# Kernel tuning notes

Hardware: AMD Instinct MI355X
Metric: run time of the kernel (lower is better)

The kernel has to match this reference:

```python
import jax, jax.numpy as jnp
import numpy as np

IN_CH = 64
OUT_CH = 64
MODES = 16
BATCH, H, W = 16, 128, 128


def setup_inputs() -> dict:
    key = jax.random.key(0)
    k1, k2, k3 = jax.random.split(key, 3)
    scale = 1.0 / (IN_CH * OUT_CH)
    x = jax.random.normal(k1, (BATCH, H, W, IN_CH), dtype=jnp.float32)
    weights_real = (scale * jax.random.normal(k2, (IN_CH, OUT_CH, MODES, MODES))).astype(jnp.float32)
    weights_imag = (scale * jax.random.normal(k3, (IN_CH, OUT_CH, MODES, MODES))).astype(jnp.float32)
    return {"x": x, "weights_real": weights_real, "weights_imag": weights_imag}


def reference(x, weights_real, weights_imag):
    # x: (b, h, w, c_in)
    b, h, w, _ = x.shape
    modes = weights_real.shape[-1]
    out_ch = weights_real.shape[1]

    xc = jnp.transpose(x, (0, 3, 1, 2))               # (b, c_in, h, w)
    x_ft = jnp.fft.rfft2(xc, norm="ortho")           # (b, c_in, h, w//2+1) complex64

    # Complex spectral weights; the torch double loop over (i, j) is exactly
    # a per-mode channel contraction over the low-frequency block.
    Wc = (weights_real + 1j * weights_imag).astype(jnp.complex64)
    out_modes = jnp.einsum("bixy,ioxy->boxy", x_ft[:, :, :modes, :modes], Wc)

    out_ft = jnp.zeros((b, out_ch, h, w // 2 + 1), dtype=jnp.complex64)
    out_ft = out_ft.at[:, :, :modes, :modes].set(out_modes)

    y = jnp.fft.irfft2(out_ft, s=(h, w), norm="ortho")  # (b, c_out, h, w)
    return jnp.transpose(y, (0, 2, 3, 1))                # (b, h, w, c_out)
```

## Files before the change

### kernel.cpp

```cpp
#include <hip/hip_runtime.h>

#define NB 16
#define NH 128
#define NW 128
#define NC 64
#define NO 64
#define NM 16

#define OFF_WTR  0
#define OFF_WTI  (OFF_WTR + 1048576)
#define OFF_AR   (OFF_WTI + 1048576)
#define OFF_AI   (OFF_AR + 2097152)
#define OFF_XR   (OFF_AI + 2097152)
#define OFF_XI   (OFF_XR + 262144)
#define OFF_OR   (OFF_XI + 262144)
#define OFF_OI   (OFF_OR + 262144)

#define R2F 0.70710678118654752f

constexpr float CQ[33] = {
  1.000000000f, 0.998795456f, 0.995184727f, 0.989176510f,
  0.980785280f, 0.970031253f, 0.956940336f, 0.941544065f,
  0.923879533f, 0.903989293f, 0.881921264f, 0.857728610f,
  0.831469612f, 0.803207531f, 0.773010453f, 0.740951125f,
  0.707106781f, 0.671558955f, 0.634393284f, 0.595699304f,
  0.555570233f, 0.514102744f, 0.471396737f, 0.427555093f,
  0.382683432f, 0.336889853f, 0.290284677f, 0.242980180f,
  0.195090322f, 0.146730474f, 0.098017140f, 0.049067674f,
  0.000000000f };

__host__ __device__ constexpr float twcos(int t) {
  t &= 127;
  return (t <= 32) ? CQ[t] : (t < 64) ? -CQ[64 - t] : (t <= 96) ? -CQ[t - 64] : CQ[128 - t];
}
__host__ __device__ constexpr float twsin(int t) { return twcos(t + 96); }

template<int T>
__device__ __forceinline__ void caccN_t(float gr, float gi, float& ar, float& ai) {
  constexpr int t = T & 127;
  if constexpr (t == 0)       { ar += gr; ai += gi; }
  else if constexpr (t == 64) { ar -= gr; ai -= gi; }
  else if constexpr (t == 32) { ar += gi; ai -= gr; }
  else if constexpr (t == 96) { ar -= gi; ai += gr; }
  else {
    constexpr float c = twcos(t), s = twsin(t);
    ar = fmaf(gr, c, fmaf(gi, s, ar));
    ai = fmaf(gi, c, fmaf(-gr, s, ai));
  }
}
template<int T>
__device__ __forceinline__ void caccP_t(float gr, float gi, float& ar, float& ai) {
  constexpr int t = T & 127;
  if constexpr (t == 0)       { ar += gr; ai += gi; }
  else if constexpr (t == 64) { ar -= gr; ai -= gi; }
  else if constexpr (t == 32) { ar -= gi; ai += gr; }
  else if constexpr (t == 96) { ar += gi; ai -= gr; }
  else {
    constexpr float c = twcos(t), s = twsin(t);
    ar = fmaf(gr, c, fmaf(-gi, s, ar));
    ai = fmaf(gi, c, fmaf(gr, s, ai));
  }
}
template<int T>
__device__ __forceinline__ void crotN_t(float& ar, float& ai) {
  constexpr int t = T & 127;
  if constexpr (t == 0) {}
  else if constexpr (t == 64) { ar = -ar; ai = -ai; }
  else if constexpr (t == 32) { const float r = ar; ar = ai; ai = -r; }
  else if constexpr (t == 96) { const float r = ar; ar = -ai; ai = r; }
  else {
    constexpr float c = twcos(t), s = twsin(t);
    const float r = ar;
    ar = fmaf(r, c, ai * s);
    ai = fmaf(ai, c, -r * s);
  }
}
template<int T>
__device__ __forceinline__ void crotP_t(float& ar, float& ai) {
  constexpr int t = T & 127;
  if constexpr (t == 0) {}
  else if constexpr (t == 64) { ar = -ar; ai = -ai; }
  else if constexpr (t == 32) { const float r = ar; ar = -ai; ai = r; }
  else if constexpr (t == 96) { const float r = ar; ar = ai;  ai = -r; }
  else {
    constexpr float c = twcos(t), s = twsin(t);
    const float r = ar;
    ar = fmaf(r, c, -(ai * s));
    ai = fmaf(ai, c, r * s);
  }
}

__global__ __launch_bounds__(256) void k_wt(const float* __restrict__ wre,
                                            const float* __restrict__ wim,
                                            float* __restrict__ wtr,
                                            float* __restrict__ wti) {
  __shared__ float buf[64 * 257];
  const int i = blockIdx.x & 63;
  const float* src = (blockIdx.x < 64) ? wre : wim;
  float* dst       = (blockIdx.x < 64) ? wtr : wti;
  const float* s = src + (size_t)i * 16384;
  for (int t = threadIdx.x; t < 16384; t += 256) {
    int o = t >> 8, kk = t & 255;
    buf[o * 257 + kk] = s[t];
  }
  __syncthreads();
  for (int t = threadIdx.x; t < 16384; t += 256) {
    int kk = t >> 6, o = t & 63;
    dst[(size_t)kk * 4096 + i * 64 + o] = buf[o * 257 + kk];
  }
}

template<int K>
__device__ __forceinline__ void k1_zeroT(float (&Tr)[16], float (&Ti)[16]) {
  if constexpr (K < 16) { Tr[K] = 0.f; Ti[K] = 0.f; k1_zeroT<K + 1>(Tr, Ti); }
}
template<int K, int P0>
__device__ __forceinline__ void k1_initR(float (&Rr)[16], float (&Ri)[16]) {
  if constexpr (K < 16) {
    constexpr int t = (K * P0) & 127;
    Rr[K] = twcos(t);
    Ri[K] = -twsin(t);
    k1_initR<K + 1, P0>(Rr, Ri);
  }
}
template<int W1>
__device__ __forceinline__ void k1_ld8(const float* xp, int w0, float (&v)[8]) {
  if constexpr (W1 < 8) {
    v[W1] = xp[(W1 * 16 + w0) * NC];
    k1_ld8<W1 + 1>(xp, w0, v);
  }
}
template<int W1>
__device__ __forceinline__ void k1_cp8(float (&a)[8], const float (&b)[8]) {
  if constexpr (W1 < 8) { a[W1] = b[W1]; k1_cp8<W1 + 1>(a, b); }
}
template<int KY>
__device__ __forceinline__ void k1_acc(float g0r, float g4r, float g1r, float g1i,
                                       float g2r, float g2i, float g3r, float g3i,
                                       float (&Tr)[16], float (&Ti)[16],
                                       float (&Rr)[16], float (&Ri)[16]) {
  if constexpr (KY < 16) {
    constexpr int p = KY & 7;
    if constexpr (p == 0 || p == 4) {
      const float gr = (p == 0) ? g0r : g4r;
      Tr[KY] = fmaf(gr, Rr[KY], Tr[KY]);
      Ti[KY] = fmaf(gr, Ri[KY], Ti[KY]);
    } else {
      float gr, gi;
      if constexpr (p == 1)      { gr = g1r; gi = g1i; }
      else if constexpr (p == 2) { gr = g2r; gi = g2i; }
      else if constexpr (p == 3) { gr = g3r; gi = g3i; }
      else if constexpr (p == 5) { gr = g3r; gi = -g3i; }
      else if constexpr (p == 6) { gr = g2r; gi = -g2i; }
      else                       { gr = g1r; gi = -g1i; }
      Tr[KY] = fmaf(gr, Rr[KY], fmaf(-gi, Ri[KY], Tr[KY]));
      Ti[KY] = fmaf(gr, Ri[KY], fmaf( gi, Rr[KY], Ti[KY]));
    }
    crotN_t<KY>(Rr[KY], Ri[KY]);
    k1_acc<KY + 1>(g0r, g4r, g1r, g1i, g2r, g2i, g3r, g3i, Tr, Ti, Rr, Ri);
  }
}
template<int K>
__device__ __forceinline__ void k1_ldswr(float* p, const float (&Tr)[16], const float (&Ti)[16]) {
  if constexpr (K < 16) {
    p[K * 64]        = Tr[K];
    p[(16 + K) * 64] = Ti[K];
    k1_ldswr<K + 1>(p, Tr, Ti);
  }
}
template<int K>
__device__ __forceinline__ void k1_ldsadd(const float* p, float (&Tr)[16], float (&Ti)[16]) {
  if constexpr (K < 16) {
    Tr[K] += p[K * 64];
    Ti[K] += p[(16 + K) * 64];
    k1_ldsadd<K + 1>(p, Tr, Ti);
  }
}
template<int KY>
__device__ __forceinline__ void k1_store(float* t1r, float* t1i,
                                         const float (&Tr)[16], const float (&Ti)[16]) {
  if constexpr (KY < 16) {
    t1r[(size_t)KY * (NH * NC)] = Tr[KY];
    t1i[(size_t)KY * (NH * NC)] = Ti[KY];
    k1_store<KY + 1>(t1r, t1i, Tr, Ti);
  }
}

__global__ __launch_bounds__(256, 4) void k1_wdft(const float* __restrict__ x,
                                                  float* __restrict__ t1r,
                                                  float* __restrict__ t1i) {
  __shared__ float lds[2][32][64];
  const int wv   = threadIdx.x >> 6;
  const int lane = threadIdx.x & 63;
  const int sq   = wv >> 1;
  const int half = wv & 1;
  const int slab = blockIdx.x * 2 + sq;
  const float* xp = x + (size_t)slab * (NW * NC) + lane;
  float Tr[16], Ti[16], Rr[16], Ri[16];
  k1_zeroT<0>(Tr, Ti);
  if (half == 0) k1_initR<0, 0>(Rr, Ri);
  else           k1_initR<0, 8>(Rr, Ri);
  float xv[8], nx[8];
  k1_ld8<0>(xp, half * 8, xv);
  for (int it = 0; it < 8; ++it) {
    const int w0 = half * 8 + it;
    if (it < 7) k1_ld8<0>(xp, w0 + 1, nx);
    const float s0 = xv[0] + xv[4], d0 = xv[0] - xv[4];
    const float s1 = xv[1] + xv[5], d1 = xv[1] - xv[5];
    const float s2 = xv[2] + xv[6], d2 = xv[2] - xv[6];
    const float s3 = xv[3] + xv[7], d3 = xv[3] - xv[7];
    const float e0 = s0 + s2, e1 = s0 - s2;
    const float f0 = s1 + s3, f1 = s1 - s3;
    const float u = R2F * (d1 - d3), v = R2F * (d1 + d3);
    const float g0r = e0 + f0;
    const float g4r = e0 - f0;
    const float g1r = d0 + u, g1i = -(d2 + v);
    const float g2r = e1,     g2i = -f1;
    const float g3r = d0 - u, g3i = d2 - v;
    k1_acc<0>(g0r, g4r, g1r, g1i, g2r, g2i, g3r, g3i, Tr, Ti, Rr, Ri);
    k1_cp8<0>(xv, nx);
  }
  float* lp = &lds[sq][0][lane];
  if (half) k1_ldswr<0>(lp, Tr, Ti);
  __syncthreads();
  if (!half) {
    k1_ldsadd<0>(lp, Tr, Ti);
    const int b = slab >> 7, h = slab & 127;
    const size_t base = ((size_t)b * 2048 + h) * NC + lane;
    k1_store<0>(t1r + base, t1i + base, Tr, Ti);
  }
}

template<int K>
__device__ __forceinline__ void k2a_zero(float (&Ar)[16], float (&Ai)[16]) {
  if constexpr (K < 16) { Ar[K] = 0.f; Ai[K] = 0.f; k2a_zero<K + 1>(Ar, Ai); }
}
template<int KX, int J>
__device__ __forceinline__ void k2a_kx(float re, float im, float (&Ar)[16], float (&Ai)[16]) {
  if constexpr (KX < 16) {
    caccN_t<(KX * J) & 127>(re, im, Ar[KX], Ai[KX]);
    k2a_kx<KX + 1, J>(re, im, Ar, Ai);
  }
}
template<int J>
__device__ __forceinline__ void k2a_j(const float* pr, const float* pi,
                                      float (&Ar)[16], float (&Ai)[16]) {
  if constexpr (J < 8) {
    const float re = pr[J * NC];
    const float im = pi[J * NC];
    k2a_kx<0, J>(re, im, Ar, Ai);
    k2a_j<J + 1>(pr, pi, Ar, Ai);
  }
}
template<int G, int KX>
__device__ __forceinline__ void k2a_rotg(float (&Ar)[16], float (&Ai)[16]) {
  if constexpr (KX < 16) {
    crotN_t<(8 * KX * G) & 127>(Ar[KX], Ai[KX]);
    k2a_rotg<G, KX + 1>(Ar, Ai);
  }
}
template<int KX>
__device__ __forceinline__ void k2a_ldsw(float* pr, float* pi,
                                         const float (&Ar)[16], const float (&Ai)[16]) {
  if constexpr (KX < 16) {
    pr[KX * 64] = Ar[KX]; pi[KX * 64] = Ai[KX];
    k2a_ldsw<KX + 1>(pr, pi, Ar, Ai);
  }
}
template<int KX>
__device__ __forceinline__ void k2a_ldsa(float* pr, float* pi,
                                         const float (&Ar)[16], const float (&Ai)[16]) {
  if constexpr (KX < 16) {
    pr[KX * 64] += Ar[KX]; pi[KX * 64] += Ai[KX];
    k2a_ldsa<KX + 1>(pr, pi, Ar, Ai);
  }
}

__global__ __launch_bounds__(1024, 4) void k2a_hdft(const float* __restrict__ t1r,
                                                    const float* __restrict__ t1i,
                                                    float* __restrict__ xre,
                                                    float* __restrict__ xim) {
  __shared__ float lpr[8][16][64];
  __shared__ float lpi[8][16][64];
  const int bk   = blockIdx.x;
  const int q    = threadIdx.x >> 6;
  const int lane = threadIdx.x & 63;
  const float* pr = t1r + (size_t)bk * (NH * NC) + (q * 8) * NC + lane;
  const float* pi = t1i + (size_t)bk * (NH * NC) + (q * 8) * NC + lane;
  float Ar[16], Ai[16];
  k2a_zero<0>(Ar, Ai);
  k2a_j<0>(pr, pi, Ar, Ai);
  switch (q) {
    case 1:  k2a_rotg<1, 0>(Ar, Ai);  break;
    case 2:  k2a_rotg<2, 0>(Ar, Ai);  break;
    case 3:  k2a_rotg<3, 0>(Ar, Ai);  break;
    case 4:  k2a_rotg<4, 0>(Ar, Ai);  break;
    case 5:  k2a_rotg<5, 0>(Ar, Ai);  break;
    case 6:  k2a_rotg<6, 0>(Ar, Ai);  break;
    case 7:  k2a_rotg<7, 0>(Ar, Ai);  break;
    case 8:  k2a_rotg<8, 0>(Ar, Ai);  break;
    case 9:  k2a_rotg<9, 0>(Ar, Ai);  break;
    case 10: k2a_rotg<10, 0>(Ar, Ai); break;
    case 11: k2a_rotg<11, 0>(Ar, Ai); break;
    case 12: k2a_rotg<12, 0>(Ar, Ai); break;
    case 13: k2a_rotg<13, 0>(Ar, Ai); break;
    case 14: k2a_rotg<14, 0>(Ar, Ai); break;
    case 15: k2a_rotg<15, 0>(Ar, Ai); break;
    default: break;
  }
  float* wpr = &lpr[q & 7][0][lane];
  float* wpi = &lpi[q & 7][0][lane];
  if (q < 8) k2a_ldsw<0>(wpr, wpi, Ar, Ai);
  __syncthreads();
  if (q >= 8) k2a_ldsa<0>(wpr, wpi, Ar, Ai);
  __syncthreads();
  const int kx = threadIdx.x >> 6;
  const int i  = threadIdx.x & 63;
  float sr = 0.f, si = 0.f;
#pragma unroll
  for (int p = 0; p < 8; ++p) { sr += lpr[p][kx][i]; si += lpi[p][kx][i]; }
  const int b = bk >> 4, ky = bk & 15;
  const size_t idx = (size_t)(kx * NM + ky) * (NB * NC) + b * NC + i;
  xre[idx] = sr;
  xim[idx] = si;
}

__global__ __launch_bounds__(512, 2) void k2b_mix(const float* __restrict__ xre,
                                                  const float* __restrict__ xim,
                                                  const float* __restrict__ wtr,
                                                  const float* __restrict__ wti,
                                                  float* __restrict__ ore,
                                                  float* __restrict__ oim) {
  __shared__ __align__(16) float lwr[4096], lwi[4096];
  __shared__ __align__(16) float lxr[1024], lxi[1024];
  const int kk = blockIdx.x;
  for (int t = threadIdx.x; t < 4096; t += 512) {
    lwr[t] = wtr[(size_t)kk * 4096 + t];
    lwi[t] = wti[(size_t)kk * 4096 + t];
  }
  for (int t = threadIdx.x; t < 1024; t += 512) {
    lxr[t] = xre[(size_t)kk * 1024 + t];
    lxi[t] = xim[(size_t)kk * 1024 + t];
  }
  __syncthreads();
  const int o  = threadIdx.x & 63;
  const int bq = threadIdx.x >> 6;
  float accr[2] = {0, 0}, acci[2] = {0, 0};
  for (int iq = 0; iq < 16; ++iq) {
    float xrv[2][4], xiv[2][4];
#pragma unroll
    for (int p = 0; p < 2; ++p) {
      const int b = bq * 2 + p;
      float4 vr = ((const float4*)lxr)[b * 16 + iq];
      float4 vi = ((const float4*)lxi)[b * 16 + iq];
      xrv[p][0] = vr.x; xrv[p][1] = vr.y; xrv[p][2] = vr.z; xrv[p][3] = vr.w;
      xiv[p][0] = vi.x; xiv[p][1] = vi.y; xiv[p][2] = vi.z; xiv[p][3] = vi.w;
    }
#pragma unroll
    for (int j = 0; j < 4; ++j) {
      const int i2 = iq * 4 + j;
      const float wr = lwr[i2 * 64 + o];
      const float wi = lwi[i2 * 64 + o];
#pragma unroll
      for (int p = 0; p < 2; ++p) {
        accr[p] = fmaf(xrv[p][j], wr, fmaf(-xiv[p][j], wi, accr[p]));
        acci[p] = fmaf(xrv[p][j], wi, fmaf(xiv[p][j], wr, acci[p]));
      }
    }
  }
#pragma unroll
  for (int p = 0; p < 2; ++p) {
    const int b = bq * 2 + p;
    ore[(size_t)kk * 1024 + b * 64 + o] = accr[p];
    oim[(size_t)kk * 1024 + b * 64 + o] = acci[p];
  }
}

__global__ __launch_bounds__(256, 2) void k3_hidft(const float* __restrict__ ore,
                                                   const float* __restrict__ oim,
                                                   float* __restrict__ t2r,
                                                   float* __restrict__ t2i) {
  const int b = blockIdx.x >> 5, hq = blockIdx.x & 31;
  const int q = threadIdx.x >> 6, lane = threadIdx.x & 63;
  const int ky0 = q * 4;
  float sc[4], ss[4];
  {
    const int h0 = 4 * hq;
    float wr = 1.f, wi = 0.f;
    if (h0 & 4)  crotP_t<4>(wr, wi);
    if (h0 & 8)  crotP_t<8>(wr, wi);
    if (h0 & 16) crotP_t<16>(wr, wi);
    if (h0 & 32) crotP_t<32>(wr, wi);
    if (h0 & 64) crotP_t<64>(wr, wi);
    sc[0] = wr; ss[0] = wi;
    crotP_t<1>(wr, wi); sc[1] = wr; ss[1] = wi;
    crotP_t<1>(wr, wi); sc[2] = wr; ss[2] = wi;
    crotP_t<1>(wr, wi); sc[3] = wr; ss[3] = wi;
  }
  float Rr[4] = {1.f, 1.f, 1.f, 1.f}, Ri[4] = {0.f, 0.f, 0.f, 0.f};
  float tr[4][4], ti[4][4];
#pragma unroll
  for (int j = 0; j < 4; ++j)
#pragma unroll
    for (int k = 0; k < 4; ++k) { tr[j][k] = 0.f; ti[j][k] = 0.f; }
  const size_t obase = (size_t)b * NO + lane;
  for (int kx = 0; kx < 16; ++kx) {
    float orv[4], oiv[4];
#pragma unroll
    for (int k = 0; k < 4; ++k) {
      const size_t idx = (size_t)(kx * 16 + ky0 + k) * (NB * NO) + obase;
      orv[k] = ore[idx];
      oiv[k] = oim[idx];
    }
#pragma unroll
    for (int j = 0; j < 4; ++j)
#pragma unroll
      for (int k = 0; k < 4; ++k) {
        tr[j][k] = fmaf(orv[k], Rr[j], fmaf(-oiv[k], Ri[j], tr[j][k]));
        ti[j][k] = fmaf(orv[k], Ri[j], fmaf( oiv[k], Rr[j], ti[j][k]));
      }
#pragma unroll
    for (int j = 0; j < 4; ++j) {
      const float nr = fmaf(Rr[j], sc[j], -(Ri[j] * ss[j]));
      const float ni = fmaf(Rr[j], ss[j], Ri[j] * sc[j]);
      Rr[j] = nr; Ri[j] = ni;
    }
  }
#pragma unroll
  for (int j = 0; j < 4; ++j) {
    const int h = hq * 4 + j;
#pragma unroll
    for (int k = 0; k < 4; ++k) {
      const int ky = ky0 + k;
      const float scale = (ky == 0 ? 1.0f : 2.0f) * (1.0f / 16384.0f);
      const size_t idx = ((size_t)(b * NH + h) * NM + ky) * NO + lane;
      t2r[idx] = tr[j][k] * scale;
      t2i[idx] = ti[j][k] * scale;
    }
  }
}

template<int KY>
__device__ __forceinline__ void k5_load(const float* pr, const float* pi,
                                        float (&Tr)[16], float (&Ti)[16]) {
  if constexpr (KY < 16) {
    Tr[KY] = pr[KY * NO];
    Ti[KY] = pi[KY * NO];
    k5_load<KY + 1>(pr, pi, Tr, Ti);
  }
}
template<int KY, int W0>
__device__ __forceinline__ void k5_u(const float (&Tr)[16], const float (&Ti)[16],
                                     float (&Ur)[8], float (&Ui)[8]) {
  if constexpr (KY < 16) {
    caccP_t<(KY * W0) & 127>(Tr[KY], Ti[KY], Ur[KY & 7], Ui[KY & 7]);
    k5_u<KY + 1, W0>(Tr, Ti, Ur, Ui);
  }
}
template<int P>
__device__ __forceinline__ void k5_uzero(float (&Ur)[8], float (&Ui)[8]) {
  if constexpr (P < 8) { Ur[P] = 0.f; Ui[P] = 0.f; k5_uzero<P + 1>(Ur, Ui); }
}
template<int W0, int W0END>
__device__ __forceinline__ void k5_w0(const float (&Tr)[16], const float (&Ti)[16],
                                      float* yp) {
  if constexpr (W0 < W0END) {
    float Ur[8], Ui[8];
    k5_uzero<0>(Ur, Ui);
    k5_u<0, W0>(Tr, Ti, Ur, Ui);
    const float A  = Ur[0], B = Ur[4];
    const float Cr = Ur[2] + Ur[6], Ci = Ui[2] - Ui[6];
    const float Dr = Ur[1] + Ur[7], Di = Ui[1] - Ui[7];
    const float Er = Ur[3] + Ur[5], Ei = Ui[3] - Ui[5];
    const float P = A + B, M = A - B;
    const float DE = Dr + Er, IE = Di - Ei;
    const float X1 = R2F * ((Dr - Di) - (Er + Ei));
    const float X3 = R2F * ((Dr + Di) - (Er - Ei));
    const float MmC = M - Ci, MpC = M + Ci, PpC = P + Cr, PmC = P - Cr;
    yp[(0 * 16 + W0) * NO] = PpC + DE;
    yp[(4 * 16 + W0) * NO] = PpC - DE;
    yp[(2 * 16 + W0) * NO] = PmC - IE;
    yp[(6 * 16 + W0) * NO] = PmC + IE;
    yp[(1 * 16 + W0) * NO] = MmC + X1;
    yp[(5 * 16 + W0) * NO] = MmC - X1;
    yp[(3 * 16 + W0) * NO] = MpC - X3;
    yp[(7 * 16 + W0) * NO] = MpC + X3;
    k5_w0<W0 + 1, W0END>(Tr, Ti, yp);
  }
}

__global__ __launch_bounds__(256, 4) void k5_widft(const float* __restrict__ t2r,
                                                   const float* __restrict__ t2i,
                                                   float* __restrict__ y) {
  const int wv   = threadIdx.x >> 6;
  const int lane = threadIdx.x & 63;
  const int sq   = wv >> 1;
  const int half = wv & 1;
  const int slab = blockIdx.x * 2 + sq;
  const float* pr = t2r + (size_t)slab * (NM * NO) + lane;
  const float* pi = t2i + (size_t)slab * (NM * NO) + lane;
  float Tr[16], Ti[16];
  k5_load<0>(pr, pi, Tr, Ti);
  float* yp = y + (size_t)slab * (NW * NO) + lane;
  if (half == 0) k5_w0<0, 8>(Tr, Ti, yp);
  else           k5_w0<8, 16>(Tr, Ti, yp);
}

extern "C" void kernel_launch(void* const* d_in, const int* in_sizes, int n_in,
                              void* d_out, int out_size, void* d_ws, size_t ws_size,
                              hipStream_t stream) {
  const float* x   = (const float*)d_in[0];
  const float* wre = (const float*)d_in[1];
  const float* wim = (const float*)d_in[2];
  float* ws  = (float*)d_ws;
  float* wtr = ws + OFF_WTR;
  float* wti = ws + OFF_WTI;
  float* ar  = ws + OFF_AR;
  float* ai  = ws + OFF_AI;
  float* xr  = ws + OFF_XR;
  float* xi  = ws + OFF_XI;
  float* orr = ws + OFF_OR;
  float* oii = ws + OFF_OI;
  float* y   = (float*)d_out;

  k_wt<<<128, 256, 0, stream>>>(wre, wim, wtr, wti);
  k1_wdft<<<1024, 256, 0, stream>>>(x, ar, ai);
  k2a_hdft<<<NB * NM, 1024, 0, stream>>>(ar, ai, xr, xi);
  k2b_mix<<<NM * NM, 512, 0, stream>>>(xr, xi, wtr, wti, orr, oii);
  k3_hidft<<<512, 256, 0, stream>>>(orr, oii, ar, ai);
  k5_widft<<<1024, 256, 0, stream>>>(ar, ai, y);
}
```

Baseline: 155.6 us.

## Fuse inverse H/W DFT kernels and drop separate weight transpose

```diff
diff --git a/kernel.cpp b/kernel.cpp
--- a/kernel.cpp
+++ b/kernel.cpp
@@ -7,9 +7,7 @@
 #define NO 64
 #define NM 16
 
-#define OFF_WTR  0
-#define OFF_WTI  (OFF_WTR + 1048576)
-#define OFF_AR   (OFF_WTI + 1048576)
+#define OFF_AR   0
 #define OFF_AI   (OFF_AR + 2097152)
 #define OFF_XR   (OFF_AI + 2097152)
 #define OFF_XI   (OFF_XR + 262144)
@@ -87,26 +85,6 @@
     const float r = ar;
     ar = fmaf(r, c, -(ai * s));
     ai = fmaf(ai, c, r * s);
-  }
-}
-
-__global__ __launch_bounds__(256) void k_wt(const float* __restrict__ wre,
-                                            const float* __restrict__ wim,
-                                            float* __restrict__ wtr,
-                                            float* __restrict__ wti) {
-  __shared__ float buf[64 * 257];
-  const int i = blockIdx.x & 63;
-  const float* src = (blockIdx.x < 64) ? wre : wim;
-  float* dst       = (blockIdx.x < 64) ? wtr : wti;
-  const float* s = src + (size_t)i * 16384;
-  for (int t = threadIdx.x; t < 16384; t += 256) {
-    int o = t >> 8, kk = t & 255;
-    buf[o * 257 + kk] = s[t];
-  }
-  __syncthreads();
-  for (int t = threadIdx.x; t < 16384; t += 256) {
-    int kk = t >> 6, o = t & 63;
-    dst[(size_t)kk * 4096 + i * 64 + o] = buf[o * 257 + kk];
   }
 }
 
@@ -327,16 +305,16 @@
 
 __global__ __launch_bounds__(512, 2) void k2b_mix(const float* __restrict__ xre,
                                                   const float* __restrict__ xim,
-                                                  const float* __restrict__ wtr,
-                                                  const float* __restrict__ wti,
+                                                  const float* __restrict__ wre,
+                                                  const float* __restrict__ wim,
                                                   float* __restrict__ ore,
                                                   float* __restrict__ oim) {
   __shared__ __align__(16) float lwr[4096], lwi[4096];
   __shared__ __align__(16) float lxr[1024], lxi[1024];
   const int kk = blockIdx.x;
   for (int t = threadIdx.x; t < 4096; t += 512) {
-    lwr[t] = wtr[(size_t)kk * 4096 + t];
-    lwi[t] = wti[(size_t)kk * 4096 + t];
+    lwr[t] = wre[(size_t)t * 256 + kk];
+    lwi[t] = wim[(size_t)t * 256 + kk];
   }
   for (int t = threadIdx.x; t < 1024; t += 512) {
     lxr[t] = xre[(size_t)kk * 1024 + t];
@@ -376,77 +354,51 @@
   }
 }
 
-__global__ __launch_bounds__(256, 2) void k3_hidft(const float* __restrict__ ore,
-                                                   const float* __restrict__ oim,
-                                                   float* __restrict__ t2r,
-                                                   float* __restrict__ t2i) {
-  const int b = blockIdx.x >> 5, hq = blockIdx.x & 31;
-  const int q = threadIdx.x >> 6, lane = threadIdx.x & 63;
-  const int ky0 = q * 4;
-  float sc[4], ss[4];
-  {
-    const int h0 = 4 * hq;
-    float wr = 1.f, wi = 0.f;
-    if (h0 & 4)  crotP_t<4>(wr, wi);
-    if (h0 & 8)  crotP_t<8>(wr, wi);
-    if (h0 & 16) crotP_t<16>(wr, wi);
-    if (h0 & 32) crotP_t<32>(wr, wi);
-    if (h0 & 64) crotP_t<64>(wr, wi);
-    sc[0] = wr; ss[0] = wi;
-    crotP_t<1>(wr, wi); sc[1] = wr; ss[1] = wi;
-    crotP_t<1>(wr, wi); sc[2] = wr; ss[2] = wi;
-    crotP_t<1>(wr, wi); sc[3] = wr; ss[3] = wi;
-  }
-  float Rr[4] = {1.f, 1.f, 1.f, 1.f}, Ri[4] = {0.f, 0.f, 0.f, 0.f};
-  float tr[4][4], ti[4][4];
-#pragma unroll
-  for (int j = 0; j < 4; ++j)
-#pragma unroll
-    for (int k = 0; k < 4; ++k) { tr[j][k] = 0.f; ti[j][k] = 0.f; }
-  const size_t obase = (size_t)b * NO + lane;
-  for (int kx = 0; kx < 16; ++kx) {
-    float orv[4], oiv[4];
-#pragma unroll
-    for (int k = 0; k < 4; ++k) {
-      const size_t idx = (size_t)(kx * 16 + ky0 + k) * (NB * NO) + obase;
-      orv[k] = ore[idx];
-      oiv[k] = oim[idx];
-    }
-#pragma unroll
-    for (int j = 0; j < 4; ++j)
-#pragma unroll
-      for (int k = 0; k < 4; ++k) {
-        tr[j][k] = fmaf(orv[k], Rr[j], fmaf(-oiv[k], Ri[j], tr[j][k]));
-        ti[j][k] = fmaf(orv[k], Ri[j], fmaf( oiv[k], Rr[j], ti[j][k]));
-      }
-#pragma unroll
-    for (int j = 0; j < 4; ++j) {
-      const float nr = fmaf(Rr[j], sc[j], -(Ri[j] * ss[j]));
-      const float ni = fmaf(Rr[j], ss[j], Ri[j] * sc[j]);
-      Rr[j] = nr; Ri[j] = ni;
-    }
-  }
-#pragma unroll
-  for (int j = 0; j < 4; ++j) {
-    const int h = hq * 4 + j;
-#pragma unroll
-    for (int k = 0; k < 4; ++k) {
-      const int ky = ky0 + k;
-      const float scale = (ky == 0 ? 1.0f : 2.0f) * (1.0f / 16384.0f);
-      const size_t idx = ((size_t)(b * NH + h) * NM + ky) * NO + lane;
-      t2r[idx] = tr[j][k] * scale;
-      t2i[idx] = ti[j][k] * scale;
-    }
-  }
-}
-
-template<int KY>
-__device__ __forceinline__ void k5_load(const float* pr, const float* pi,
+template<int K>
+__device__ __forceinline__ void k35_zero(float (&Tr)[16], float (&Ti)[16]) {
+  if constexpr (K < 16) { Tr[K] = 0.f; Ti[K] = 0.f; k35_zero<K + 1>(Tr, Ti); }
+}
+template<int KY, int KYEND>
+__device__ __forceinline__ void k35_ld(const float* orp, const float* oip,
+                                       float (&orv)[16], float (&oiv)[16]) {
+  if constexpr (KY < KYEND) {
+    orv[KY] = orp[KY * (NB * NO)];
+    oiv[KY] = oip[KY * (NB * NO)];
+    k35_ld<KY + 1, KYEND>(orp, oip, orv, oiv);
+  }
+}
+template<int KY, int KYEND>
+__device__ __forceinline__ void k35_acc(const float (&orv)[16], const float (&oiv)[16],
+                                        float Rr, float Ri,
                                         float (&Tr)[16], float (&Ti)[16]) {
-  if constexpr (KY < 16) {
-    Tr[KY] = pr[KY * NO];
-    Ti[KY] = pi[KY * NO];
-    k5_load<KY + 1>(pr, pi, Tr, Ti);
+  if constexpr (KY < KYEND) {
+    Tr[KY] = fmaf(orv[KY], Rr, fmaf(-oiv[KY], Ri, Tr[KY]));
+    Ti[KY] = fmaf(orv[KY], Ri, fmaf( oiv[KY], Rr, Ti[KY]));
+    k35_acc<KY + 1, KYEND>(orv, oiv, Rr, Ri, Tr, Ti);
+  }
+}
+template<int K>
+__device__ __forceinline__ void k35_ldswr(float* p, const float (&Tr)[16], const float (&Ti)[16]) {
+  if constexpr (K < 16) {
+    p[K * 64]        = Tr[K];
+    p[(16 + K) * 64] = Ti[K];
+    k35_ldswr<K + 1>(p, Tr, Ti);
+  }
+}
+template<int K>
+__device__ __forceinline__ void k35_ldsadd(const float* p, float (&Tr)[16], float (&Ti)[16]) {
+  if constexpr (K < 16) {
+    Tr[K] += p[K * 64];
+    Ti[K] += p[(16 + K) * 64];
+    k35_ldsadd<K + 1>(p, Tr, Ti);
+  }
+}
+template<int K>
+__device__ __forceinline__ void k35_scale(float (&Tr)[16], float (&Ti)[16]) {
+  if constexpr (K < 16) {
+    constexpr float sc = (K == 0 ? 1.0f : 2.0f) * (1.0f / 16384.0f);
+    Tr[K] *= sc; Ti[K] *= sc;
+    k35_scale<K + 1>(Tr, Ti);
   }
 }
 template<int KY, int W0>
@@ -489,21 +441,56 @@
   }
 }
 
-__global__ __launch_bounds__(256, 4) void k5_widft(const float* __restrict__ t2r,
-                                                   const float* __restrict__ t2i,
-                                                   float* __restrict__ y) {
+__global__ __launch_bounds__(256, 4) void k35_inv(const float* __restrict__ ore,
+                                                  const float* __restrict__ oim,
+                                                  float* __restrict__ y) {
+  __shared__ float lds[2][2][32][64];
   const int wv   = threadIdx.x >> 6;
   const int lane = threadIdx.x & 63;
   const int sq   = wv >> 1;
-  const int half = wv & 1;
+  const int kh   = wv & 1;
   const int slab = blockIdx.x * 2 + sq;
-  const float* pr = t2r + (size_t)slab * (NM * NO) + lane;
-  const float* pi = t2i + (size_t)slab * (NM * NO) + lane;
+  const int b = slab >> 7, h = slab & 127;
+  float c1 = 1.f, s1 = 0.f;
+  if (h & 1)  crotP_t<1>(c1, s1);
+  if (h & 2)  crotP_t<2>(c1, s1);
+  if (h & 4)  crotP_t<4>(c1, s1);
+  if (h & 8)  crotP_t<8>(c1, s1);
+  if (h & 16) crotP_t<16>(c1, s1);
+  if (h & 32) crotP_t<32>(c1, s1);
+  if (h & 64) crotP_t<64>(c1, s1);
+  float Rr = 1.f, Ri = 0.f;
+  if (kh) {
+    if (h & 1) crotP_t<8>(Rr, Ri);
+    if (h & 2) crotP_t<16>(Rr, Ri);
+    if (h & 4) crotP_t<32>(Rr, Ri);
+    if (h & 8) crotP_t<64>(Rr, Ri);
+  }
   float Tr[16], Ti[16];
-  k5_load<0>(pr, pi, Tr, Ti);
+  k35_zero<0>(Tr, Ti);
+  const float* orp = ore + (size_t)(kh * 8) * (NM * NB * NO) + b * NO + lane;
+  const float* oip = oim + (size_t)(kh * 8) * (NM * NB * NO) + b * NO + lane;
+  for (int kx = 0; kx < 8; ++kx) {
+    float orv[16], oiv[16];
+    k35_ld<0, 8>(orp, oip, orv, oiv);
+    k35_acc<0, 8>(orv, oiv, Rr, Ri, Tr, Ti);
+    k35_ld<8, 16>(orp, oip, orv, oiv);
+    k35_acc<8, 16>(orv, oiv, Rr, Ri, Tr, Ti);
+    const float nr = fmaf(Rr, c1, -(Ri * s1));
+    const float ni = fmaf(Rr, s1, Ri * c1);
+    Rr = nr; Ri = ni;
+    orp += NM * NB * NO;
+    oip += NM * NB * NO;
+  }
+  float* wp = &lds[sq][kh][0][lane];
+  k35_ldswr<0>(wp, Tr, Ti);
+  __syncthreads();
+  const float* rp = &lds[sq][kh ^ 1][0][lane];
+  k35_ldsadd<0>(rp, Tr, Ti);
+  k35_scale<0>(Tr, Ti);
   float* yp = y + (size_t)slab * (NW * NO) + lane;
-  if (half == 0) k5_w0<0, 8>(Tr, Ti, yp);
-  else           k5_w0<8, 16>(Tr, Ti, yp);
+  if (kh == 0) k5_w0<0, 8>(Tr, Ti, yp);
+  else         k5_w0<8, 16>(Tr, Ti, yp);
 }
 
 extern "C" void kernel_launch(void* const* d_in, const int* in_sizes, int n_in,
@@ -513,8 +500,6 @@
   const float* wre = (const float*)d_in[1];
   const float* wim = (const float*)d_in[2];
   float* ws  = (float*)d_ws;
-  float* wtr = ws + OFF_WTR;
-  float* wti = ws + OFF_WTI;
   float* ar  = ws + OFF_AR;
   float* ai  = ws + OFF_AI;
   float* xr  = ws + OFF_XR;
@@ -523,10 +508,8 @@
   float* oii = ws + OFF_OI;
   float* y   = (float*)d_out;
 
-  k_wt<<<128, 256, 0, stream>>>(wre, wim, wtr, wti);
   k1_wdft<<<1024, 256, 0, stream>>>(x, ar, ai);
   k2a_hdft<<<NB * NM, 1024, 0, stream>>>(ar, ai, xr, xi);
-  k2b_mix<<<NM * NM, 512, 0, stream>>>(xr, xi, wtr, wti, orr, oii);
-  k3_hidft<<<512, 256, 0, stream>>>(orr, oii, ar, ai);
-  k5_widft<<<1024, 256, 0, stream>>>(ar, ai, y);
-}
+  k2b_mix<<<NM * NM, 512, 0, stream>>>(xr, xi, wre, wim, orr, oii);
+  k35_inv<<<1024, 256, 0, stream>>>(orr, oii, y);
+}
```

After: 159.7 us. 2.6% more time.
